# Optimization experiments

Measured on AMD Instinct MI355X. Metric: run time of the kernel, lower is better.

The kernel has to match this reference:

```python
import jax, jax.numpy as jnp
import numpy as np

N = 200000   # active voxel sites
G = 80       # voxel grid extent per axis
K = 27       # 3x3x3 kernel offsets
CIN = 64
COUT = 128
EPS = 1e-5


def _build_rulebook(seed=0):
    """Submanifold 3x3x3 rulebook: for each offset k and output site i,
    in_idx[k,i] = index of neighbor site (or 0 if absent),
    out_idx[k,i] = i (or N = dummy row if neighbor absent)."""
    rng = np.random.default_rng(seed)
    lin = rng.choice(G ** 3, size=N, replace=False).astype(np.int64)
    lut = np.full(G ** 3, -1, dtype=np.int64)
    lut[lin] = np.arange(N)
    cx, cy, cz = lin // (G * G), (lin // G) % G, lin % G
    offs = [(dx, dy, dz) for dx in (-1, 0, 1) for dy in (-1, 0, 1) for dz in (-1, 0, 1)]
    in_idx = np.zeros((K, N), np.int32)
    out_idx = np.full((K, N), N, np.int32)
    ar = np.arange(N, dtype=np.int32)
    for k, (dx, dy, dz) in enumerate(offs):
        nx, ny, nz = cx + dx, cy + dy, cz + dz
        ok = (nx >= 0) & (nx < G) & (ny >= 0) & (ny < G) & (nz >= 0) & (nz < G)
        nb_lin = np.where(ok, nx * G * G + ny * G + nz, 0)
        j = lut[nb_lin]
        valid = ok & (j >= 0)
        in_idx[k] = np.where(valid, j, 0).astype(np.int32)
        out_idx[k] = np.where(valid, ar, N)
    return jnp.asarray(in_idx), jnp.asarray(out_idx)


def setup_inputs() -> dict:
    key = jax.random.key(0)
    ks = jax.random.split(key, 8)
    in_idx, out_idx = _build_rulebook(0)
    s1 = 1.0 / np.sqrt(CIN * K)
    s2 = 1.0 / np.sqrt(COUT * K)
    ss = 1.0 / np.sqrt(CIN)
    return {
        "feats": jax.random.normal(ks[0], (N, CIN), jnp.float32),
        "in_idx": in_idx,
        "out_idx": out_idx,
        "W1": jax.random.normal(ks[1], (K, CIN, COUT), jnp.float32) * s1,
        "g1": jnp.ones((COUT,), jnp.float32) + 0.1 * jax.random.normal(ks[2], (COUT,), jnp.float32),
        "b1": 0.1 * jax.random.normal(ks[3], (COUT,), jnp.float32),
        "W2": jax.random.normal(ks[4], (K, COUT, COUT), jnp.float32) * s2,
        "g2": jnp.ones((COUT,), jnp.float32) + 0.1 * jax.random.normal(ks[5], (COUT,), jnp.float32),
        "b2": 0.1 * jax.random.normal(ks[6], (COUT,), jnp.float32),
        "Wsc": jax.random.normal(ks[7], (CIN, COUT), jnp.float32) * ss,
        "gsc": jnp.ones((COUT,), jnp.float32),
        "bsc": jnp.zeros((COUT,), jnp.float32),
    }


def _spconv(feats, W, in_idx, out_idx):
    """Rulebook gather-GEMM-scatter sparse conv. feats [N,Cin], W [K,Cin,Cout]."""
    cout = W.shape[-1]
    out = jnp.zeros((N + 1, cout), feats.dtype)  # row N = dummy for padded pairs
    for k in range(K):  # fixed small structural loop over kernel offsets
        out = out.at[out_idx[k]].add(feats[in_idx[k]] @ W[k])
    return out[:N]


def _bn(x, gamma, beta):
    # training-mode BatchNorm over the site dimension (biased variance)
    m = jnp.mean(x, axis=0)
    v = jnp.var(x, axis=0)
    return (x - m) * jax.lax.rsqrt(v + EPS) * gamma + beta


def reference(feats, in_idx, out_idx, W1, g1, b1, W2, g2, b2, Wsc, gsc, bsc):
    h = jax.nn.relu(_bn(_spconv(feats, W1, in_idx, out_idx), g1, b1))
    h = _bn(_spconv(h, W2, in_idx, out_idx), g2, b2)
    sc = _bn(feats @ Wsc, gsc, bsc)  # 1x1 sparse conv == per-site linear
    return jax.nn.relu(h + sc)
```

## Files before the change

kernel.cpp:

```cpp
#include <hip/hip_runtime.h>

#define NS 200000
#define NK 27
#define NB 782
#define NBSC 1563
#define EPSV 1e-5f

typedef __bf16 bf16x8 __attribute__((ext_vector_type(8)));
typedef float f32x4 __attribute__((ext_vector_type(4)));
typedef unsigned short u16;
typedef u16 u16x8 __attribute__((ext_vector_type(8)));
typedef u16 u16x4 __attribute__((ext_vector_type(4)));
typedef unsigned u32;

__device__ __forceinline__ u16 f2bf(float f) {
  union { float f; unsigned u; } v; v.f = f;
  unsigned r = v.u + 0x7fffu + ((v.u >> 16) & 1u);
  return (u16)(r >> 16);
}
__device__ __forceinline__ float bf2f(u16 u) {
  union { unsigned u; float f; } v; v.u = ((unsigned)u) << 16;
  return v.f;
}

__global__ void k_prep_x(const float* __restrict__ feats, u16* __restrict__ Xbf,
                         float* __restrict__ stats) {
  long i = (long)blockIdx.x * 256 + threadIdx.x;
  if (i < 768) stats[i] = 0.f;
  const long total = (long)NS * 64;
  if (i < total) Xbf[i] = f2bf(feats[i]);
}

__global__ void k_prep_gidx(const int* __restrict__ in_idx, const int* __restrict__ out_idx,
                            int* __restrict__ gidx) {
  long i = (long)blockIdx.x * 256 + threadIdx.x;
  if (i < (long)NK * NS) gidx[i] = (out_idx[i] != NS) ? in_idx[i] : NS;
}

__global__ void k_pack_w(const float* __restrict__ W1, const float* __restrict__ W2,
                         const float* __restrict__ Wsc, u16* __restrict__ Wp1,
                         u16* __restrict__ Wp2, u16* __restrict__ Wpsc) {
  int i = blockIdx.x * 256 + threadIdx.x;
  const int n1 = NK * 64 * 128, n2 = NK * 128 * 128, n3 = 64 * 128;
  const float* src; u16* dst; int f, S, C;
  if (i < n1)            { src = W1;  dst = Wp1;  f = i;            S = 2; C = 64; }
  else if (i < n1 + n2)  { src = W2;  dst = Wp2;  f = i - n1;       S = 4; C = 128; }
  else if (i < n1 + n2 + n3) { src = Wsc; dst = Wpsc; f = i - n1 - n2; S = 2; C = 64; }
  else return;
  int j = f & 7, l = (f >> 3) & 63, cf = (f >> 9) & 7;
  int rest = f >> 12;
  int s = rest % S, k = rest / S;
  int kk = s * 32 + (l >> 4) * 8 + j;
  dst[f] = f2bf(src[(k * C + kk) * 128 + cf * 16 + (l & 15)]);
}

template <int C>
__global__ __launch_bounds__(256, 2) void k_conv(
    const u16* __restrict__ X, const u16* __restrict__ Wp,
    const int* __restrict__ gidx,
    u16* __restrict__ Y, float* __restrict__ partial) {
  constexpr int S = C / 32;
  constexpr int SLICE = C * 128;
  constexpr int NST = C / 16;
  constexpr int WAITN = NST + 4;
  __shared__ alignas(16) u16 Wbuf[2 * SLICE];
  __shared__ float red[1024];

  const int t = threadIdx.x, w = t >> 6, l = t & 63;
  const int lr = l & 15, lh = l >> 4;
  const int rowbase = blockIdx.x * 256 + w * 64;
  const int laneoff = l * 8;

  int rc[4]; bool ok[4];
  #pragma unroll
  for (int m = 0; m < 4; ++m) {
    int r = rowbase + m * 16 + lr;
    ok[m] = r < NS;
    rc[m] = ok[m] ? r : 0;
  }

  auto stage = [&](int k, int p) {
    #pragma unroll
    for (int i = 0; i < NST; ++i) {
      const u16* g = Wp + k * SLICE + (w * NST + i) * 512 + laneoff;
      u16* d = &Wbuf[p * SLICE + (w * NST + i) * 512];
      __builtin_amdgcn_global_load_lds(
          (const __attribute__((address_space(1))) u32*)g,
          (__attribute__((address_space(3))) u32*)d, 16, 0, 0);
    }
  };
  auto loadidx = [&](int k, int (&dst)[4]) {
    #pragma unroll
    for (int m = 0; m < 4; ++m) {
      int v = gidx[k * NS + rc[m]];
      dst[m] = ok[m] ? v : NS;
    }
  };
  auto gather = [&](const int (&src)[4], bf16x8 (&a)[4][S]) {
    #pragma unroll
    for (int m = 0; m < 4; ++m) {
      #pragma unroll
      for (int s = 0; s < S; ++s) a[m][s] = bf16x8{};
      if (src[m] != NS) {
        const u16* rowp = X + src[m] * C + lh * 8;
        #pragma unroll
        for (int s = 0; s < S; ++s)
          a[m][s] = *reinterpret_cast<const bf16x8*>(rowp + s * 32);
      }
    }
  };
  auto compute = [&](int p, const bf16x8 (&a)[4][S], f32x4 (&ac)[4][8]) {
    __builtin_amdgcn_s_setprio(1);
    #pragma unroll
    for (int s = 0; s < S; ++s)
      #pragma unroll
      for (int cf = 0; cf < 8; ++cf) {
        bf16x8 b = *reinterpret_cast<const bf16x8*>(
            &Wbuf[p * SLICE + (s * 8 + cf) * 512 + laneoff]);
        #pragma unroll
        for (int m = 0; m < 4; ++m)
          ac[m][cf] = __builtin_amdgcn_mfma_f32_16x16x32_bf16(a[m][s], b, ac[m][cf], 0, 0, 0);
      }
    __builtin_amdgcn_s_setprio(0);
  };

  f32x4 acc[4][8];
  #pragma unroll
  for (int m = 0; m < 4; ++m)
    #pragma unroll
    for (int cf = 0; cf < 8; ++cf) acc[m][cf] = (f32x4){0.f, 0.f, 0.f, 0.f};

  bf16x8 av[4][S];
  int sv0[4], sv1[4];

  loadidx(0, sv0);
  stage(0, 0);
  loadidx(1, sv1);
  gather(sv0, av);

  #pragma unroll 1
  for (int k = 0; k < NK - 1; k += 2) {
    stage(k + 1, 1);
    loadidx(k + 2, sv0);
    asm volatile("s_waitcnt vmcnt(%0)\n\ts_barrier" :: "i"(WAITN) : "memory");
    compute(0, av, acc);
    gather(sv1, av);
    asm volatile("s_waitcnt lgkmcnt(0)\n\ts_barrier" ::: "memory");
    stage(k + 2, 0);
    { int kn = (k + 3 < NK) ? k + 3 : NK - 1; loadidx(kn, sv1); }
    asm volatile("s_waitcnt vmcnt(%0)\n\ts_barrier" :: "i"(WAITN) : "memory");
    compute(1, av, acc);
    gather(sv0, av);
    asm volatile("s_waitcnt lgkmcnt(0)\n\ts_barrier" ::: "memory");
  }
  asm volatile("s_waitcnt vmcnt(0)\n\ts_barrier" ::: "memory");
  compute(0, av, acc);

  #pragma unroll
  for (int m = 0; m < 4; ++m)
    #pragma unroll
    for (int cf = 0; cf < 8; ++cf) {
      int ch = cf * 16 + lr;
      #pragma unroll
      for (int r = 0; r < 4; ++r) {
        int row = rowbase + m * 16 + lh * 4 + r;
        if (row < NS) Y[row * 128 + ch] = f2bf(acc[m][cf][r]);
      }
    }
  #pragma unroll
  for (int cf = 0; cf < 8; ++cf) {
    float s = 0.f, q = 0.f;
    #pragma unroll
    for (int m = 0; m < 4; ++m)
      #pragma unroll
      for (int r = 0; r < 4; ++r) { float v = acc[m][cf][r]; s += v; q += v * v; }
    s += __shfl_xor(s, 16); s += __shfl_xor(s, 32);
    q += __shfl_xor(q, 16); q += __shfl_xor(q, 32);
    if (lh == 0) {
      red[w * 256 + cf * 16 + lr] = s;
      red[w * 256 + 128 + cf * 16 + lr] = q;
    }
  }
  __syncthreads();
  if (t < 256)
    partial[blockIdx.x * 256 + t] =
        red[t] + red[256 + t] + red[512 + t] + red[768 + t];
}

__global__ __launch_bounds__(256, 2) void k_sc(
    const u16* __restrict__ X, const u16* __restrict__ Wpsc,
    u16* __restrict__ SCb, float* __restrict__ partial) {
  __shared__ float red[1024];
  const int t = threadIdx.x, w = t >> 6, l = t & 63;
  const int lr = l & 15, lh = l >> 4;
  const int rowbase = blockIdx.x * 128 + w * 32;
  const int laneoff = l * 8;

  bf16x8 ai[2][2];
  #pragma unroll
  for (int m = 0; m < 2; ++m) {
    int r = rowbase + m * 16 + lr;
    #pragma unroll
    for (int s = 0; s < 2; ++s) ai[m][s] = bf16x8{};
    if (r < NS) {
      const u16* rowp = X + r * 64 + lh * 8;
      ai[m][0] = *reinterpret_cast<const bf16x8*>(rowp);
      ai[m][1] = *reinterpret_cast<const bf16x8*>(rowp + 32);
    }
  }
  f32x4 acc[2][8];
  #pragma unroll
  for (int m = 0; m < 2; ++m)
    #pragma unroll
    for (int cf = 0; cf < 8; ++cf) acc[m][cf] = (f32x4){0.f, 0.f, 0.f, 0.f};
  #pragma unroll
  for (int s = 0; s < 2; ++s)
    #pragma unroll
    for (int cf = 0; cf < 8; ++cf) {
      bf16x8 b = *reinterpret_cast<const bf16x8*>(Wpsc + (s * 8 + cf) * 512 + laneoff);
      acc[0][cf] = __builtin_amdgcn_mfma_f32_16x16x32_bf16(ai[0][s], b, acc[0][cf], 0, 0, 0);
      acc[1][cf] = __builtin_amdgcn_mfma_f32_16x16x32_bf16(ai[1][s], b, acc[1][cf], 0, 0, 0);
    }
  #pragma unroll
  for (int m = 0; m < 2; ++m)
    #pragma unroll
    for (int cf = 0; cf < 8; ++cf) {
      int ch = cf * 16 + lr;
      #pragma unroll
      for (int r = 0; r < 4; ++r) {
        int row = rowbase + m * 16 + lh * 4 + r;
        if (row < NS) SCb[row * 128 + ch] = f2bf(acc[m][cf][r]);
      }
    }
  #pragma unroll
  for (int cf = 0; cf < 8; ++cf) {
    float s = 0.f, q = 0.f;
    #pragma unroll
    for (int m = 0; m < 2; ++m)
      #pragma unroll
      for (int r = 0; r < 4; ++r) { float v = acc[m][cf][r]; s += v; q += v * v; }
    s += __shfl_xor(s, 16); s += __shfl_xor(s, 32);
    q += __shfl_xor(q, 16); q += __shfl_xor(q, 32);
    if (lh == 0) {
      red[w * 256 + cf * 16 + lr] = s;
      red[w * 256 + 128 + cf * 16 + lr] = q;
    }
  }
  __syncthreads();
  if (t < 256)
    partial[blockIdx.x * 256 + t] =
        red[t] + red[256 + t] + red[512 + t] + red[768 + t];
}

__global__ void k_red1(const float* __restrict__ part, float* __restrict__ tmp,
                       int pc, int nrows) {
  int c = blockIdx.x * 256 + threadIdx.x;
  float s = 0.f;
  for (int r = blockIdx.y; r < nrows; r += 32) s += part[(long)r * pc + c];
  tmp[(long)blockIdx.y * pc + c] = s;
}
__global__ void k_red2(const float* __restrict__ tmp, float* __restrict__ out, int pc) {
  int c = blockIdx.x * 256 + threadIdx.x;
  float s = 0.f;
  #pragma unroll
  for (int r = 0; r < 32; ++r) s += tmp[(long)r * pc + c];
  out[c] = s;
}

__global__ void k_bnrelu(const u16* __restrict__ Y1, const float* __restrict__ stats,
                         const float* __restrict__ g, const float* __restrict__ b,
                         u16* __restrict__ H) {
  long i8 = (long)blockIdx.x * 256 + threadIdx.x;
  const long tot = (long)NS * 16;
  if (i8 >= tot) return;
  int ch0 = ((int)i8 & 15) * 8;
  u16x8 y = *reinterpret_cast<const u16x8*>(Y1 + i8 * 8);
  u16x8 o;
  #pragma unroll
  for (int e = 0; e < 8; ++e) {
    int ch = ch0 + e;
    float m = stats[ch] * (1.f / NS);
    float var = stats[128 + ch] * (1.f / NS) - m * m;
    float a = g[ch] * rsqrtf(var + EPSV);
    float bb = b[ch] - m * a;
    float h = bf2f(y[e]) * a + bb;
    o[e] = f2bf(h > 0.f ? h : 0.f);
  }
  *reinterpret_cast<u16x8*>(H + i8 * 8) = o;
}

__global__ void k_final(const u16* __restrict__ Y2, const u16* __restrict__ SCb,
                        const float* __restrict__ stats,
                        const float* __restrict__ g2, const float* __restrict__ b2,
                        const float* __restrict__ gsc, const float* __restrict__ bsc,
                        float* __restrict__ out) {
  long i4 = (long)blockIdx.x * 256 + threadIdx.x;
  if (i4 >= (long)NS * 32) return;
  int ch0 = ((int)i4 & 31) * 4;
  u16x4 y = *reinterpret_cast<const u16x4*>(Y2 + i4 * 4);
  u16x4 s = *reinterpret_cast<const u16x4*>(SCb + i4 * 4);
  f32x4 o;
  #pragma unroll
  for (int e = 0; e < 4; ++e) {
    int ch = ch0 + e;
    float m2 = stats[512 + ch] * (1.f / NS);
    float v2 = stats[640 + ch] * (1.f / NS) - m2 * m2;
    float a2 = g2[ch] * rsqrtf(v2 + EPSV);
    float msc = stats[256 + ch] * (1.f / NS);
    float vsc = stats[384 + ch] * (1.f / NS) - msc * msc;
    float asc = gsc[ch] * rsqrtf(vsc + EPSV);
    float val = bf2f(y[e]) * a2 + (b2[ch] - m2 * a2)
              + bf2f(s[e]) * asc + (bsc[ch] - msc * asc);
    o[e] = val > 0.f ? val : 0.f;
  }
  *reinterpret_cast<f32x4*>(out + i4 * 4) = o;
}

extern "C" void kernel_launch(void* const* d_in, const int* in_sizes, int n_in,
                              void* d_out, int out_size, void* d_ws, size_t ws_size,
                              hipStream_t stream) {
  const float* feats = (const float*)d_in[0];
  const int* in_idx  = (const int*)d_in[1];
  const int* out_idx = (const int*)d_in[2];
  const float* W1  = (const float*)d_in[3];
  const float* g1  = (const float*)d_in[4];
  const float* b1  = (const float*)d_in[5];
  const float* W2  = (const float*)d_in[6];
  const float* g2  = (const float*)d_in[7];
  const float* b2  = (const float*)d_in[8];
  const float* Wsc = (const float*)d_in[9];
  const float* gsc = (const float*)d_in[10];
  const float* bsc = (const float*)d_in[11];

  char* ws = (char*)d_ws;
  size_t off = 0;
  auto alloc = [&](size_t bytes) {
    void* p = ws + off; off += (bytes + 255) & ~(size_t)255; return p;
  };
  float* stats = (float*)alloc(768 * 4);
  float* rtmp  = (float*)alloc(32 * 512 * 4);
  u16* Xbf  = (u16*)alloc((size_t)NS * 64 * 2);
  u16* SCbf = (u16*)alloc((size_t)NS * 128 * 2);
  u16* Hbf  = (u16*)alloc((size_t)NS * 128 * 2);
  u16* Y2bf = (u16*)alloc((size_t)NS * 128 * 2);
  u16* Wp1  = (u16*)alloc((size_t)NK * 64 * 128 * 2);
  u16* Wp2  = (u16*)alloc((size_t)NK * 128 * 128 * 2);
  u16* Wpsc = (u16*)alloc((size_t)64 * 128 * 2);
  u16* Y1bf = (u16*)d_out;
  int* gidx = (int*)((char*)d_out + (size_t)NS * 128 * 2);
  float* part1  = (float*)Y2bf;
  float* partsc = part1 + (size_t)NB * 256;
  float* part2  = (float*)Xbf;

  hipLaunchKernelGGL(k_prep_x, dim3(50000), dim3(256), 0, stream, feats, Xbf, stats);
  hipLaunchKernelGGL(k_prep_gidx, dim3((NK * NS + 255) / 256), dim3(256), 0, stream,
                     in_idx, out_idx, gidx);
  hipLaunchKernelGGL(k_pack_w, dim3(2624), dim3(256), 0, stream, W1, W2, Wsc, Wp1, Wp2, Wpsc);
  hipLaunchKernelGGL(k_sc, dim3(NBSC), dim3(256), 0, stream, Xbf, Wpsc, SCbf, partsc);
  hipLaunchKernelGGL(k_red1, dim3(1, 32), dim3(256), 0, stream, partsc, rtmp, 256, NBSC);
  hipLaunchKernelGGL(k_red2, dim3(1), dim3(256), 0, stream, rtmp, stats + 256, 256);
  hipLaunchKernelGGL((k_conv<64>), dim3(NB), dim3(256), 0, stream,
                     Xbf, Wp1, gidx, Y1bf, part1);
  hipLaunchKernelGGL(k_red1, dim3(1, 32), dim3(256), 0, stream, part1, rtmp, 256, NB);
  hipLaunchKernelGGL(k_red2, dim3(1), dim3(256), 0, stream, rtmp, stats, 256);
  hipLaunchKernelGGL(k_bnrelu, dim3(12500), dim3(256), 0, stream, Y1bf, stats, g1, b1, Hbf);
  hipLaunchKernelGGL((k_conv<128>), dim3(NB), dim3(256), 0, stream,
                     Hbf, Wp2, gidx, Y2bf, part2);
  hipLaunchKernelGGL(k_red1, dim3(1, 32), dim3(256), 0, stream, part2, rtmp, 256, NB);
  hipLaunchKernelGGL(k_red2, dim3(1), dim3(256), 0, stream, rtmp, stats + 512, 256);
  hipLaunchKernelGGL(k_final, dim3(25000), dim3(256), 0, stream,
                     Y2bf, SCbf, stats, g2, b2, gsc, bsc, (float*)d_out);
}
```

Measured before the change: 442.1 us.

## Halve conv block rows and split K into 64-channel slices for higher occupancy

The sparse conv kernel now processes 128 rows per block (32 per wave) instead of 256, doubling the grid and raising launch bounds to 4 blocks per CU. The weight slice staged in LDS is fixed at 64 input channels, so the 128-channel conv splits each offset into two half-K stages, with a rewritten, fully unrolled double-buffered pipeline. This is meant to cut register and LDS pressure and improve latency hiding of the gathers. In exchange, each weight tile is reused over fewer rows, so there are more barriers and more weight traffic per output row.

Result: slower. 520.6 us (+17.7%).

```diff
diff --git a/kernel.cpp b/kernel.cpp
--- a/kernel.cpp
+++ b/kernel.cpp
@@ -2,8 +2,7 @@
 
 #define NS 200000
 #define NK 27
-#define NB 782
-#define NBSC 1563
+#define NB 1563
 #define EPSV 1e-5f
 
 typedef __bf16 bf16x8 __attribute__((ext_vector_type(8)));
@@ -55,109 +54,130 @@
 }
 
 template <int C>
-__global__ __launch_bounds__(256, 2) void k_conv(
+__global__ __launch_bounds__(256, 4) void k_conv(
     const u16* __restrict__ X, const u16* __restrict__ Wp,
     const int* __restrict__ gidx,
     u16* __restrict__ Y, float* __restrict__ partial) {
-  constexpr int S = C / 32;
-  constexpr int SLICE = C * 128;
-  constexpr int NST = C / 16;
-  constexpr int WAITN = NST + 4;
-  __shared__ alignas(16) u16 Wbuf[2 * SLICE];
+  constexpr int H = C / 64;
+  constexpr int SL = 64 * 128;
+  __shared__ alignas(16) u16 Wbuf[2 * SL];
   __shared__ float red[1024];
 
   const int t = threadIdx.x, w = t >> 6, l = t & 63;
   const int lr = l & 15, lh = l >> 4;
-  const int rowbase = blockIdx.x * 256 + w * 64;
+  const int rowbase = blockIdx.x * 128 + w * 32;
   const int laneoff = l * 8;
 
-  int rc[4]; bool ok[4];
-  #pragma unroll
-  for (int m = 0; m < 4; ++m) {
+  int rc[2]; bool ok[2];
+  #pragma unroll
+  for (int m = 0; m < 2; ++m) {
     int r = rowbase + m * 16 + lr;
     ok[m] = r < NS;
     rc[m] = ok[m] ? r : 0;
   }
 
-  auto stage = [&](int k, int p) {
-    #pragma unroll
-    for (int i = 0; i < NST; ++i) {
-      const u16* g = Wp + k * SLICE + (w * NST + i) * 512 + laneoff;
-      u16* d = &Wbuf[p * SLICE + (w * NST + i) * 512];
+  auto stage = [&](int v, int p) {
+    #pragma unroll
+    for (int i = 0; i < 4; ++i) {
+      const u16* g = Wp + (long)v * SL + (w * 4 + i) * 512 + laneoff;
+      u16* d = &Wbuf[p * SL + (w * 4 + i) * 512];
       __builtin_amdgcn_global_load_lds(
           (const __attribute__((address_space(1))) u32*)g,
           (__attribute__((address_space(3))) u32*)d, 16, 0, 0);
     }
   };
-  auto loadidx = [&](int k, int (&dst)[4]) {
-    #pragma unroll
-    for (int m = 0; m < 4; ++m) {
+  auto loadidx = [&](int k, int (&dst)[2]) {
+    #pragma unroll
+    for (int m = 0; m < 2; ++m) {
       int v = gidx[k * NS + rc[m]];
       dst[m] = ok[m] ? v : NS;
     }
   };
-  auto gather = [&](const int (&src)[4], bf16x8 (&a)[4][S]) {
-    #pragma unroll
-    for (int m = 0; m < 4; ++m) {
-      #pragma unroll
-      for (int s = 0; s < S; ++s) a[m][s] = bf16x8{};
+  auto gather = [&](const int (&src)[2], int h, bf16x8 (&a)[2][2]) {
+    #pragma unroll
+    for (int m = 0; m < 2; ++m) {
+      a[m][0] = bf16x8{}; a[m][1] = bf16x8{};
       if (src[m] != NS) {
-        const u16* rowp = X + src[m] * C + lh * 8;
-        #pragma unroll
-        for (int s = 0; s < S; ++s)
-          a[m][s] = *reinterpret_cast<const bf16x8*>(rowp + s * 32);
+        const u16* rowp = X + (long)src[m] * C + h * 64 + lh * 8;
+        a[m][0] = *reinterpret_cast<const bf16x8*>(rowp);
+        a[m][1] = *reinterpret_cast<const bf16x8*>(rowp + 32);
       }
     }
   };
-  auto compute = [&](int p, const bf16x8 (&a)[4][S], f32x4 (&ac)[4][8]) {
+  auto compute = [&](int p, const bf16x8 (&a)[2][2], f32x4 (&ac)[2][8]) {
     __builtin_amdgcn_s_setprio(1);
     #pragma unroll
-    for (int s = 0; s < S; ++s)
+    for (int si = 0; si < 2; ++si)
       #pragma unroll
       for (int cf = 0; cf < 8; ++cf) {
         bf16x8 b = *reinterpret_cast<const bf16x8*>(
-            &Wbuf[p * SLICE + (s * 8 + cf) * 512 + laneoff]);
-        #pragma unroll
-        for (int m = 0; m < 4; ++m)
-          ac[m][cf] = __builtin_amdgcn_mfma_f32_16x16x32_bf16(a[m][s], b, ac[m][cf], 0, 0, 0);
+            &Wbuf[p * SL + (si * 8 + cf) * 512 + laneoff]);
+        ac[0][cf] = __builtin_amdgcn_mfma_f32_16x16x32_bf16(a[0][si], b, ac[0][cf], 0, 0, 0);
+        ac[1][cf] = __builtin_amdgcn_mfma_f32_16x16x32_bf16(a[1][si], b, ac[1][cf], 0, 0, 0);
       }
     __builtin_amdgcn_s_setprio(0);
   };
 
-  f32x4 acc[4][8];
-  #pragma unroll
-  for (int m = 0; m < 4; ++m)
+#define WAITB(N) asm volatile("s_waitcnt vmcnt(%0)\n\ts_barrier" :: "i"(N) : "memory")
+#define LGB      asm volatile("s_waitcnt lgkmcnt(0)\n\ts_barrier" ::: "memory")
+
+  f32x4 acc[2][8];
+  #pragma unroll
+  for (int m = 0; m < 2; ++m)
     #pragma unroll
     for (int cf = 0; cf < 8; ++cf) acc[m][cf] = (f32x4){0.f, 0.f, 0.f, 0.f};
 
-  bf16x8 av[4][S];
-  int sv0[4], sv1[4];
+  bf16x8 av[2][2];
+  int sv0[2], sv1[2];
 
   loadidx(0, sv0);
   stage(0, 0);
   loadidx(1, sv1);
-  gather(sv0, av);
-
-  #pragma unroll 1
-  for (int k = 0; k < NK - 1; k += 2) {
-    stage(k + 1, 1);
-    loadidx(k + 2, sv0);
-    asm volatile("s_waitcnt vmcnt(%0)\n\ts_barrier" :: "i"(WAITN) : "memory");
-    compute(0, av, acc);
-    gather(sv1, av);
-    asm volatile("s_waitcnt lgkmcnt(0)\n\ts_barrier" ::: "memory");
-    stage(k + 2, 0);
-    { int kn = (k + 3 < NK) ? k + 3 : NK - 1; loadidx(kn, sv1); }
-    asm volatile("s_waitcnt vmcnt(%0)\n\ts_barrier" :: "i"(WAITN) : "memory");
-    compute(1, av, acc);
-    gather(sv0, av);
-    asm volatile("s_waitcnt lgkmcnt(0)\n\ts_barrier" ::: "memory");
-  }
-  asm volatile("s_waitcnt vmcnt(0)\n\ts_barrier" ::: "memory");
-  compute(0, av, acc);
-
-  #pragma unroll
-  for (int m = 0; m < 4; ++m)
+  gather(sv0, 0, av);
+
+  if constexpr (H == 2) {
+    #pragma unroll 1
+    for (int k = 0; k < 24; k += 2) {
+      const int v = 2 * k;
+      stage(v + 1, 1);
+      WAITB(4);  compute(0, av, acc); gather(sv0, 1, av); LGB;
+      stage(v + 2, 0); loadidx(k + 2, sv0);
+      WAITB(6);  compute(1, av, acc); gather(sv1, 0, av); LGB;
+      stage(v + 3, 1);
+      WAITB(4);  compute(0, av, acc); gather(sv1, 1, av); LGB;
+      stage(v + 4, 0); loadidx(k + 3, sv1);
+      WAITB(6);  compute(1, av, acc); gather(sv0, 0, av); LGB;
+    }
+    stage(49, 1);
+    WAITB(4);  compute(0, av, acc); gather(sv0, 1, av); LGB;
+    stage(50, 0); loadidx(26, sv0);
+    WAITB(6);  compute(1, av, acc); gather(sv1, 0, av); LGB;
+    stage(51, 1);
+    WAITB(4);  compute(0, av, acc); gather(sv1, 1, av); LGB;
+    stage(52, 0);
+    WAITB(4);  compute(1, av, acc); gather(sv0, 0, av); LGB;
+    stage(53, 1);
+    WAITB(4);  compute(0, av, acc); gather(sv0, 1, av); LGB;
+    WAITB(0);  compute(1, av, acc);
+  } else {
+    #pragma unroll 1
+    for (int k = 0; k < 24; k += 2) {
+      stage(k + 1, 1); loadidx(k + 2, sv0);
+      WAITB(6);  compute(0, av, acc); gather(sv1, 0, av); LGB;
+      stage(k + 2, 0); loadidx(k + 3, sv1);
+      WAITB(6);  compute(1, av, acc); gather(sv0, 0, av); LGB;
+    }
+    stage(25, 1); loadidx(26, sv0);
+    WAITB(6);  compute(0, av, acc); gather(sv1, 0, av); LGB;
+    stage(26, 0);
+    WAITB(4);  compute(1, av, acc); gather(sv0, 0, av); LGB;
+    WAITB(0);  compute(0, av, acc);
+  }
+#undef WAITB
+#undef LGB
+
+  #pragma unroll
+  for (int m = 0; m < 2; ++m)
     #pragma unroll
     for (int cf = 0; cf < 8; ++cf) {
       int ch = cf * 16 + lr;
@@ -171,7 +191,7 @@
   for (int cf = 0; cf < 8; ++cf) {
     float s = 0.f, q = 0.f;
     #pragma unroll
-    for (int m = 0; m < 4; ++m)
+    for (int m = 0; m < 2; ++m)
       #pragma unroll
       for (int r = 0; r < 4; ++r) { float v = acc[m][cf][r]; s += v; q += v * v; }
     s += __shfl_xor(s, 16); s += __shfl_xor(s, 32);
@@ -356,8 +376,8 @@
   hipLaunchKernelGGL(k_prep_gidx, dim3((NK * NS + 255) / 256), dim3(256), 0, stream,
                      in_idx, out_idx, gidx);
   hipLaunchKernelGGL(k_pack_w, dim3(2624), dim3(256), 0, stream, W1, W2, Wsc, Wp1, Wp2, Wpsc);
-  hipLaunchKernelGGL(k_sc, dim3(NBSC), dim3(256), 0, stream, Xbf, Wpsc, SCbf, partsc);
-  hipLaunchKernelGGL(k_red1, dim3(1, 32), dim3(256), 0, stream, partsc, rtmp, 256, NBSC);
+  hipLaunchKernelGGL(k_sc, dim3(NB), dim3(256), 0, stream, Xbf, Wpsc, SCbf, partsc);
+  hipLaunchKernelGGL(k_red1, dim3(1, 32), dim3(256), 0, stream, partsc, rtmp, 256, NB);
   hipLaunchKernelGGL(k_red2, dim3(1), dim3(256), 0, stream, rtmp, stats + 256, 256);
   hipLaunchKernelGGL((k_conv<64>), dim3(NB), dim3(256), 0, stream,
                      Xbf, Wp1, gidx, Y1bf, part1);
```

## Split conv tiles across output-channel halves and use zero dummy row for gathers

Applied to the files above, without the earlier changes.

The conv kernel now uses 128-row blocks with four waves arranged 2x2 over rows and output-channel halves. Each wave holds a 4x4 accumulator set instead of 4x8, and weights are staged in fixed 8192-element slices, with the Cin=128 case split into two K-halves per offset. Launch bounds go up to 3 blocks per CU. A zeroed dummy row N is appended to X and H so that missing neighbours gather zeros without a branch. The aim is more blocks per CU and no divergent gather path, at the cost of gathering each input row twice (once per channel-half wave) and more barriers per offset.

New measurement: 657.7 us. 1.49x slower.

```diff
diff --git a/kernel.cpp b/kernel.cpp
--- a/kernel.cpp
+++ b/kernel.cpp
@@ -2,8 +2,7 @@
 
 #define NS 200000
 #define NK 27
-#define NB 782
-#define NBSC 1563
+#define NB 1563
 #define EPSV 1e-5f
 
 typedef __bf16 bf16x8 __attribute__((ext_vector_type(8)));
@@ -27,8 +26,11 @@
                          float* __restrict__ stats) {
   long i = (long)blockIdx.x * 256 + threadIdx.x;
   if (i < 768) stats[i] = 0.f;
-  const long total = (long)NS * 64;
-  if (i < total) Xbf[i] = f2bf(feats[i]);
+  const long total = (long)(NS + 1) * 64;
+  if (i < total) {
+    long row = i >> 6;
+    Xbf[i] = (row < NS) ? f2bf(feats[i]) : (u16)0;
+  }
 }
 
 __global__ void k_prep_gidx(const int* __restrict__ in_idx, const int* __restrict__ out_idx,
@@ -54,21 +56,22 @@
   dst[f] = f2bf(src[(k * C + kk) * 128 + cf * 16 + (l & 15)]);
 }
 
+#define WAITB(N) asm volatile("s_waitcnt vmcnt(%0)\n\ts_barrier" :: "i"(N) : "memory")
+#define LGB      asm volatile("s_waitcnt lgkmcnt(0)\n\ts_barrier" ::: "memory")
+
 template <int C>
-__global__ __launch_bounds__(256, 2) void k_conv(
+__global__ __launch_bounds__(256, 3) void k_conv(
     const u16* __restrict__ X, const u16* __restrict__ Wp,
     const int* __restrict__ gidx,
     u16* __restrict__ Y, float* __restrict__ partial) {
-  constexpr int S = C / 32;
-  constexpr int SLICE = C * 128;
-  constexpr int NST = C / 16;
-  constexpr int WAITN = NST + 4;
-  __shared__ alignas(16) u16 Wbuf[2 * SLICE];
+  constexpr int SL = 8192;
+  __shared__ alignas(16) u16 Wbuf[2 * SL];
   __shared__ float red[1024];
 
   const int t = threadIdx.x, w = t >> 6, l = t & 63;
   const int lr = l & 15, lh = l >> 4;
-  const int rowbase = blockIdx.x * 256 + w * 64;
+  const int wm = w >> 1, wn = w & 1;
+  const int rowbase = blockIdx.x * 128 + wm * 64;
   const int laneoff = l * 8;
 
   int rc[4]; bool ok[4];
@@ -79,11 +82,11 @@
     rc[m] = ok[m] ? r : 0;
   }
 
-  auto stage = [&](int k, int p) {
-    #pragma unroll
-    for (int i = 0; i < NST; ++i) {
-      const u16* g = Wp + k * SLICE + (w * NST + i) * 512 + laneoff;
-      u16* d = &Wbuf[p * SLICE + (w * NST + i) * 512];
+  auto stage = [&](int v, int p) {
+    #pragma unroll
+    for (int i = 0; i < 4; ++i) {
+      const u16* g = Wp + (long)v * SL + (w * 4 + i) * 512 + laneoff;
+      u16* d = &Wbuf[p * SL + (w * 4 + i) * 512];
       __builtin_amdgcn_global_load_lds(
           (const __attribute__((address_space(1))) u32*)g,
           (__attribute__((address_space(3))) u32*)d, 16, 0, 0);
@@ -92,99 +95,111 @@
   auto loadidx = [&](int k, int (&dst)[4]) {
     #pragma unroll
     for (int m = 0; m < 4; ++m) {
-      int v = gidx[k * NS + rc[m]];
+      int v = gidx[(long)k * NS + rc[m]];
       dst[m] = ok[m] ? v : NS;
     }
   };
-  auto gather = [&](const int (&src)[4], bf16x8 (&a)[4][S]) {
+  auto gather = [&](const int (&src)[4], int hoff, bf16x8 (&a)[4][2]) {
     #pragma unroll
     for (int m = 0; m < 4; ++m) {
-      #pragma unroll
-      for (int s = 0; s < S; ++s) a[m][s] = bf16x8{};
-      if (src[m] != NS) {
-        const u16* rowp = X + src[m] * C + lh * 8;
-        #pragma unroll
-        for (int s = 0; s < S; ++s)
-          a[m][s] = *reinterpret_cast<const bf16x8*>(rowp + s * 32);
-      }
-    }
-  };
-  auto compute = [&](int p, const bf16x8 (&a)[4][S], f32x4 (&ac)[4][8]) {
+      const u16* rowp = X + (long)src[m] * C + hoff + lh * 8;
+      a[m][0] = *reinterpret_cast<const bf16x8*>(rowp);
+      a[m][1] = *reinterpret_cast<const bf16x8*>(rowp + 32);
+    }
+  };
+  auto compute = [&](int p, const bf16x8 (&a)[4][2], f32x4 (&ac)[4][4]) {
     __builtin_amdgcn_s_setprio(1);
     #pragma unroll
-    for (int s = 0; s < S; ++s)
-      #pragma unroll
-      for (int cf = 0; cf < 8; ++cf) {
+    for (int si = 0; si < 2; ++si)
+      #pragma unroll
+      for (int nf = 0; nf < 4; ++nf) {
         bf16x8 b = *reinterpret_cast<const bf16x8*>(
-            &Wbuf[p * SLICE + (s * 8 + cf) * 512 + laneoff]);
+            &Wbuf[p * SL + (si * 8 + wn * 4 + nf) * 512 + laneoff]);
         #pragma unroll
         for (int m = 0; m < 4; ++m)
-          ac[m][cf] = __builtin_amdgcn_mfma_f32_16x16x32_bf16(a[m][s], b, ac[m][cf], 0, 0, 0);
+          ac[m][nf] = __builtin_amdgcn_mfma_f32_16x16x32_bf16(a[m][si], b, ac[m][nf], 0, 0, 0);
       }
     __builtin_amdgcn_s_setprio(0);
   };
 
-  f32x4 acc[4][8];
+  f32x4 acc[4][4];
   #pragma unroll
   for (int m = 0; m < 4; ++m)
     #pragma unroll
-    for (int cf = 0; cf < 8; ++cf) acc[m][cf] = (f32x4){0.f, 0.f, 0.f, 0.f};
-
-  bf16x8 av[4][S];
+    for (int nf = 0; nf < 4; ++nf) acc[m][nf] = (f32x4){0.f, 0.f, 0.f, 0.f};
+
+  bf16x8 av[4][2];
   int sv0[4], sv1[4];
 
-  loadidx(0, sv0);
-  stage(0, 0);
-  loadidx(1, sv1);
-  gather(sv0, av);
-
-  #pragma unroll 1
-  for (int k = 0; k < NK - 1; k += 2) {
-    stage(k + 1, 1);
-    loadidx(k + 2, sv0);
-    asm volatile("s_waitcnt vmcnt(%0)\n\ts_barrier" :: "i"(WAITN) : "memory");
-    compute(0, av, acc);
-    gather(sv1, av);
-    asm volatile("s_waitcnt lgkmcnt(0)\n\ts_barrier" ::: "memory");
-    stage(k + 2, 0);
-    { int kn = (k + 3 < NK) ? k + 3 : NK - 1; loadidx(kn, sv1); }
-    asm volatile("s_waitcnt vmcnt(%0)\n\ts_barrier" :: "i"(WAITN) : "memory");
-    compute(1, av, acc);
-    gather(sv0, av);
-    asm volatile("s_waitcnt lgkmcnt(0)\n\ts_barrier" ::: "memory");
-  }
-  asm volatile("s_waitcnt vmcnt(0)\n\ts_barrier" ::: "memory");
-  compute(0, av, acc);
+  if constexpr (C == 64) {
+    loadidx(0, sv0);
+    loadidx(1, sv1);
+    stage(0, 0);
+    gather(sv0, 0, av);
+    #pragma unroll 1
+    for (int k = 0; k < 26; k += 2) {
+      stage(k + 1, 1); loadidx(k + 2, sv0);
+      WAITB(8); compute(0, av, acc); gather(sv1, 0, av); LGB;
+      stage(k + 2, 0); loadidx(k + 3 < NK ? k + 3 : NK - 1, sv1);
+      WAITB(8); compute(1, av, acc); gather(sv0, 0, av); LGB;
+    }
+    stage(26, 1); loadidx(26, sv0);
+    WAITB(8); compute(0, av, acc);
+  } else {
+    loadidx(0, sv0);
+    loadidx(1, sv1);
+    stage(0, 0);
+    gather(sv0, 0, av);
+    #pragma unroll 1
+    for (int kk = 0; kk < 26; kk += 2) {
+      const int v0 = 2 * kk;
+      stage(v0 + 1, 1);
+      WAITB(4); compute(0, av, acc); gather(sv0, 64, av); LGB;
+      stage(v0 + 2, 0); loadidx(kk + 2, sv0);
+      WAITB(8); compute(1, av, acc); gather(sv1, 0, av); LGB;
+      stage(v0 + 3, 1);
+      WAITB(4); compute(0, av, acc); gather(sv1, 64, av); LGB;
+      stage(v0 + 4, 0); loadidx(kk + 3 < NK ? kk + 3 : NK - 1, sv1);
+      WAITB(8); compute(1, av, acc); gather(sv0, 0, av); LGB;
+    }
+    stage(53, 1);
+    WAITB(4); compute(0, av, acc); gather(sv0, 64, av); LGB;
+    stage(53, 0); loadidx(26, sv1);
+    WAITB(8); compute(1, av, acc);
+  }
 
   #pragma unroll
   for (int m = 0; m < 4; ++m)
     #pragma unroll
-    for (int cf = 0; cf < 8; ++cf) {
-      int ch = cf * 16 + lr;
+    for (int nf = 0; nf < 4; ++nf) {
+      int ch = wn * 64 + nf * 16 + lr;
       #pragma unroll
       for (int r = 0; r < 4; ++r) {
         int row = rowbase + m * 16 + lh * 4 + r;
-        if (row < NS) Y[row * 128 + ch] = f2bf(acc[m][cf][r]);
+        if (row < NS) Y[row * 128 + ch] = f2bf(acc[m][nf][r]);
       }
     }
   #pragma unroll
-  for (int cf = 0; cf < 8; ++cf) {
+  for (int nf = 0; nf < 4; ++nf) {
     float s = 0.f, q = 0.f;
     #pragma unroll
     for (int m = 0; m < 4; ++m)
       #pragma unroll
-      for (int r = 0; r < 4; ++r) { float v = acc[m][cf][r]; s += v; q += v * v; }
+      for (int r = 0; r < 4; ++r) { float v = acc[m][nf][r]; s += v; q += v * v; }
     s += __shfl_xor(s, 16); s += __shfl_xor(s, 32);
     q += __shfl_xor(q, 16); q += __shfl_xor(q, 32);
     if (lh == 0) {
-      red[w * 256 + cf * 16 + lr] = s;
-      red[w * 256 + 128 + cf * 16 + lr] = q;
+      red[w * 128 + nf * 16 + lr] = s;
+      red[512 + w * 128 + nf * 16 + lr] = q;
     }
   }
   __syncthreads();
-  if (t < 256)
-    partial[blockIdx.x * 256 + t] =
-        red[t] + red[256 + t] + red[512 + t] + red[768 + t];
+  if (t < 256) {
+    int isq = t >> 7, ch = t & 127;
+    int wnc = ch >> 6, cin = ch & 63;
+    partial[(long)blockIdx.x * 256 + t] =
+        red[isq * 512 + wnc * 128 + cin] + red[isq * 512 + (2 + wnc) * 128 + cin];
+  }
 }
 
 __global__ __launch_bounds__(256, 2) void k_sc(
@@ -200,13 +215,10 @@
   #pragma unroll
   for (int m = 0; m < 2; ++m) {
     int r = rowbase + m * 16 + lr;
-    #pragma unroll
-    for (int s = 0; s < 2; ++s) ai[m][s] = bf16x8{};
-    if (r < NS) {
-      const u16* rowp = X + r * 64 + lh * 8;
-      ai[m][0] = *reinterpret_cast<const bf16x8*>(rowp);
-      ai[m][1] = *reinterpret_cast<const bf16x8*>(rowp + 32);
-    }
+    long src = (r < NS) ? r : NS;
+    const u16* rowp = X + src * 64 + lh * 8;
+    ai[m][0] = *reinterpret_cast<const bf16x8*>(rowp);
+    ai[m][1] = *reinterpret_cast<const bf16x8*>(rowp + 32);
   }
   f32x4 acc[2][8];
   #pragma unroll
@@ -248,7 +260,7 @@
   }
   __syncthreads();
   if (t < 256)
-    partial[blockIdx.x * 256 + t] =
+    partial[(long)blockIdx.x * 256 + t] =
         red[t] + red[256 + t] + red[512 + t] + red[768 + t];
 }
 
@@ -271,20 +283,26 @@
                          const float* __restrict__ g, const float* __restrict__ b,
                          u16* __restrict__ H) {
   long i8 = (long)blockIdx.x * 256 + threadIdx.x;
-  const long tot = (long)NS * 16;
+  const long tot = (long)(NS + 1) * 16;
   if (i8 >= tot) return;
-  int ch0 = ((int)i8 & 15) * 8;
-  u16x8 y = *reinterpret_cast<const u16x8*>(Y1 + i8 * 8);
+  long row = i8 >> 4;
   u16x8 o;
-  #pragma unroll
-  for (int e = 0; e < 8; ++e) {
-    int ch = ch0 + e;
-    float m = stats[ch] * (1.f / NS);
-    float var = stats[128 + ch] * (1.f / NS) - m * m;
-    float a = g[ch] * rsqrtf(var + EPSV);
-    float bb = b[ch] - m * a;
-    float h = bf2f(y[e]) * a + bb;
-    o[e] = f2bf(h > 0.f ? h : 0.f);
+  if (row < NS) {
+    int ch0 = ((int)i8 & 15) * 8;
+    u16x8 y = *reinterpret_cast<const u16x8*>(Y1 + i8 * 8);
+    #pragma unroll
+    for (int e = 0; e < 8; ++e) {
+      int ch = ch0 + e;
+      float m = stats[ch] * (1.f / NS);
+      float var = stats[128 + ch] * (1.f / NS) - m * m;
+      float a = g[ch] * rsqrtf(var + EPSV);
+      float bb = b[ch] - m * a;
+      float h = bf2f(y[e]) * a + bb;
+      o[e] = f2bf(h > 0.f ? h : 0.f);
+    }
+  } else {
+    #pragma unroll
+    for (int e = 0; e < 8; ++e) o[e] = (u16)0;
   }
   *reinterpret_cast<u16x8*>(H + i8 * 8) = o;
 }
@@ -339,9 +357,9 @@
   };
   float* stats = (float*)alloc(768 * 4);
   float* rtmp  = (float*)alloc(32 * 512 * 4);
-  u16* Xbf  = (u16*)alloc((size_t)NS * 64 * 2);
+  u16* Xbf  = (u16*)alloc((size_t)(NS + 1) * 64 * 2);
   u16* SCbf = (u16*)alloc((size_t)NS * 128 * 2);
-  u16* Hbf  = (u16*)alloc((size_t)NS * 128 * 2);
+  u16* Hbf  = (u16*)alloc((size_t)(NS + 1) * 128 * 2);
   u16* Y2bf = (u16*)alloc((size_t)NS * 128 * 2);
   u16* Wp1  = (u16*)alloc((size_t)NK * 64 * 128 * 2);
   u16* Wp2  = (u16*)alloc((size_t)NK * 128 * 128 * 2);
@@ -352,18 +370,18 @@
   float* partsc = part1 + (size_t)NB * 256;
   float* part2  = (float*)Xbf;
 
-  hipLaunchKernelGGL(k_prep_x, dim3(50000), dim3(256), 0, stream, feats, Xbf, stats);
+  hipLaunchKernelGGL(k_prep_x, dim3(50001), dim3(256), 0, stream, feats, Xbf, stats);
   hipLaunchKernelGGL(k_prep_gidx, dim3((NK * NS + 255) / 256), dim3(256), 0, stream,
                      in_idx, out_idx, gidx);
   hipLaunchKernelGGL(k_pack_w, dim3(2624), dim3(256), 0, stream, W1, W2, Wsc, Wp1, Wp2, Wpsc);
-  hipLaunchKernelGGL(k_sc, dim3(NBSC), dim3(256), 0, stream, Xbf, Wpsc, SCbf, partsc);
-  hipLaunchKernelGGL(k_red1, dim3(1, 32), dim3(256), 0, stream, partsc, rtmp, 256, NBSC);
+  hipLaunchKernelGGL(k_sc, dim3(NB), dim3(256), 0, stream, Xbf, Wpsc, SCbf, partsc);
+  hipLaunchKernelGGL(k_red1, dim3(1, 32), dim3(256), 0, stream, partsc, rtmp, 256, NB);
   hipLaunchKernelGGL(k_red2, dim3(1), dim3(256), 0, stream, rtmp, stats + 256, 256);
   hipLaunchKernelGGL((k_conv<64>), dim3(NB), dim3(256), 0, stream,
                      Xbf, Wp1, gidx, Y1bf, part1);
   hipLaunchKernelGGL(k_red1, dim3(1, 32), dim3(256), 0, stream, part1, rtmp, 256, NB);
   hipLaunchKernelGGL(k_red2, dim3(1), dim3(256), 0, stream, rtmp, stats, 256);
-  hipLaunchKernelGGL(k_bnrelu, dim3(12500), dim3(256), 0, stream, Y1bf, stats, g1, b1, Hbf);
+  hipLaunchKernelGGL(k_bnrelu, dim3(12501), dim3(256), 0, stream, Y1bf, stats, g1, b1, Hbf);
   hipLaunchKernelGGL((k_conv<128>), dim3(NB), dim3(256), 0, stream,
                      Hbf, Wp2, gidx, Y2bf, part2);
   hipLaunchKernelGGL(k_red1, dim3(1, 32), dim3(256), 0, stream, part2, rtmp, 256, NB);
```
